# Kernel optimization log

Hardware: AMD Instinct MI355X
Metric: run time of the kernel (lower is better)

The kernel has to match this reference:

```python
import jax, jax.numpy as jnp
import numpy as np

EPS = 1e-5
B, NPB, G = 8, 12500, 64
N = B * NPB
N_EMB, NI, NF = 256, 128, 64
C = NI // 2  # 64


def _bn_relu(x, g, b):
    m = jnp.mean(x, axis=0)
    v = jnp.mean((x - m) ** 2, axis=0)
    return jax.nn.relu(g * (x - m) * jax.lax.rsqrt(v + EPS) + b)


def setup_inputs() -> dict:
    rng = np.random.default_rng(0)
    # unique voxel coords per batch in a 64^3 grid
    coords = np.concatenate([
        np.stack(np.unravel_index(rng.choice(G ** 3, NPB, replace=False), (G, G, G)), axis=1)
        for _ in range(B)
    ], axis=0).astype(np.int64)  # [N,3]
    batch_idx = np.repeat(np.arange(B), NPB).astype(np.int64)
    keys = ((batch_idx * G + coords[:, 0]) * G + coords[:, 1]) * G + coords[:, 2]
    order = np.argsort(keys)
    skeys = keys[order]
    offs = np.array([[dx, dy, dz] for dx in (-1, 0, 1) for dy in (-1, 0, 1) for dz in (-1, 0, 1)], np.int64)
    nbr = np.full((27, N), -1, np.int32)  # rulebook: input idx feeding each output per offset
    for k in range(27):
        nc = coords + offs[k]
        inb = np.all((nc >= 0) & (nc < G), axis=1)
        q = ((batch_idx * G + nc[:, 0]) * G + nc[:, 1]) * G + nc[:, 2]
        pos = np.clip(np.searchsorted(skeys, q), 0, N - 1)
        hit = inb & (skeys[pos] == q)
        nbr[k] = np.where(hit, order[pos], -1).astype(np.int32)

    key = jax.random.key(0)
    ks = jax.random.split(key, 8)
    s1 = 1.0 / np.sqrt(NI)
    s3 = 1.0 / np.sqrt(27 * C)
    su = 1.0 / np.sqrt(C)
    st = 1.0 / np.sqrt(N_EMB)
    return {
        "feats": jax.random.normal(ks[0], (N, NI), jnp.float32),
        "t": jax.random.normal(ks[1], (B, N_EMB), jnp.float32),
        "w_fuse": jax.random.normal(ks[2], (NI, C), jnp.float32) * s1,
        "g1": jnp.ones((C,), jnp.float32), "b1": jnp.zeros((C,), jnp.float32),
        "w_temb": jax.random.normal(ks[3], (N_EMB, C), jnp.float32) * st,
        "b_temb": jnp.zeros((C,), jnp.float32),
        "w3": jax.random.normal(ks[4], (27, C, C), jnp.float32) * s3,
        "g2": jnp.ones((C,), jnp.float32), "b2": jnp.zeros((C,), jnp.float32),
        "wup": jax.random.normal(ks[5], (8, C, NF), jnp.float32) * su,
        "g3": jnp.ones((NF,), jnp.float32), "b3": jnp.zeros((NF,), jnp.float32),
        "batch_idx": jnp.asarray(batch_idx, jnp.int32),
        "nbr": jnp.asarray(nbr),
    }


def reference(feats, t, w_fuse, g1, b1, w_temb, b_temb, w3, g2, b2, wup, g3, b3, batch_idx, nbr):
    # feature_fusion: 1x1 sparse conv == per-point GEMM, then BN + ReLU
    h = _bn_relu(feats @ w_fuse, g1, b1)  # [N, C]
    # time embedding injected per point via batch index
    emb = jax.nn.silu(t) @ w_temb + b_temb  # [B, C]
    h = h + emb[batch_idx]
    # 3x3x3 submanifold sparse conv: gather-GEMM-scatter per kernel offset
    n = h.shape[0]
    out = jnp.zeros_like(h)
    for k in range(nbr.shape[0]):  # fixed 27 offsets
        idx = nbr[k]
        valid = (idx >= 0)[:, None]
        g_k = jnp.where(valid, h[jnp.clip(idx, 0, n - 1)], 0.0)
        out = out + g_k @ w3[k]
    h2 = _bn_relu(out, g2, b2)  # [N, C]
    # transposed conv k=2 s=2: each input spawns 8 unique children -> per-offset GEMM
    up = jnp.einsum('nc,kcf->nkf', h2, wup).reshape(n * wup.shape[0], wup.shape[2])  # [8N, NF]
    return _bn_relu(up, g3, b3)
```

## Files before the change

### kernel.cpp

```cpp
#include <hip/hip_runtime.h>

#define EPSV 1e-5f

typedef __attribute__((ext_vector_type(8))) short short8;
typedef __attribute__((ext_vector_type(4))) short s16x4;
typedef __attribute__((ext_vector_type(4))) float f32x4;
typedef unsigned short ushort_t;

__device__ inline ushort_t f2bf(float f) {
    unsigned int x = __builtin_bit_cast(unsigned int, f);
    unsigned int r = (x + 0x7fffu + ((x >> 16) & 1u)) >> 16;
    return (ushort_t)r;
}
__device__ inline float bf2f(ushort_t u) {
    return __builtin_bit_cast(float, (unsigned int)u << 16);
}

__global__ __launch_bounds__(256) void k_prep(
    const float* __restrict__ w_fuse, const float* __restrict__ w3,
    const float* __restrict__ wup,
    const float* __restrict__ tin, const float* __restrict__ w_temb,
    const float* __restrict__ b_temb, float* __restrict__ emb,
    ushort_t* __restrict__ wfuset2, ushort_t* __restrict__ w3t2,
    ushort_t* __restrict__ wupt, ushort_t* __restrict__ wupt2) {
    if (blockIdx.x == 720) {
        __shared__ float st[8 * 256];
        int t = threadIdx.x;
        for (int i = t; i < 2048; i += 256) { float v = tin[i]; st[i] = v / (1.f + __expf(-v)); }
        __syncthreads();
        for (int p = t; p < 512; p += 256) {
            int bb = p >> 6, c = p & 63;
            float acc = b_temb[c];
            for (int e = 0; e < 256; e++) acc += st[bb * 256 + e] * w_temb[e * 64 + c];
            emb[bb * 64 + c] = acc;
        }
        return;
    }
    int i = blockIdx.x * 256 + threadIdx.x;
    if (i < 8192) {
        int kk = i & 127, ln = (i >> 7) & 15, j = i >> 11;
        wfuset2[i] = f2bf(w_fuse[kk * 64 + 4 * ln + j]);
    } else if (i < 118784) {
        int p = i - 8192;
        int kk = p & 63, ln = (p >> 6) & 15, j = (p >> 10) & 3, k = p >> 12;
        w3t2[p] = f2bf(w3[k * 4096 + kk * 64 + 4 * ln + j]);
    } else if (i < 151552) {
        int p = i - 118784;
        int uk = p >> 12, r = p & 4095, f = r >> 6, c = r & 63;
        wupt[p] = f2bf(wup[uk * 4096 + c * 64 + f]);
    } else if (i < 184320) {
        int p = i - 151552;
        int kk = p & 63, ln = (p >> 6) & 15, j = (p >> 10) & 3, uk = p >> 12;
        wupt2[p] = f2bf(wup[uk * 4096 + kk * 64 + 4 * ln + j]);
    }
}

__global__ __launch_bounds__(256) void k_gemm_fuse(
    const float* __restrict__ feats, const ushort_t* __restrict__ wfuset2,
    ushort_t* __restrict__ T, float* __restrict__ partialT, int npts) {
    __shared__ float sm[4][128];
    int t = threadIdx.x, bid = blockIdx.x;
    int lane = t & 63, w = t >> 6, q = lane >> 4, ln = lane & 15;
    int rbase = bid * 64 + w * 16;
    int row = rbase + ln;
    bool rv = row < npts;
    short8 afr[4];
#pragma unroll
    for (int s = 0; s < 4; s++) {
        short8 v = (short8)0;
        if (rv) {
            const float* src = feats + (size_t)row * 128 + s * 32 + q * 8;
            float4 a = *(const float4*)src;
            float4 b = *(const float4*)(src + 4);
            ushort_t u[8] = {f2bf(a.x), f2bf(a.y), f2bf(a.z), f2bf(a.w),
                             f2bf(b.x), f2bf(b.y), f2bf(b.z), f2bf(b.w)};
            v = *(short8*)u;
        }
        afr[s] = v;
    }
    f32x4 acc[4];
#pragma unroll
    for (int j = 0; j < 4; j++) acc[j] = (f32x4)0.f;
#pragma unroll
    for (int s = 0; s < 4; s++)
#pragma unroll
        for (int j = 0; j < 4; j++) {
            short8 bfr = *(const short8*)&wfuset2[j * 2048 + ln * 128 + s * 32 + q * 8];
            acc[j] = __builtin_amdgcn_mfma_f32_16x16x32_bf16(afr[s], bfr, acc[j], 0, 0, 0);
        }
    float ps[4] = {0, 0, 0, 0}, pq[4] = {0, 0, 0, 0};
#pragma unroll
    for (int r = 0; r < 4; r++) {
        int rr = rbase + q * 4 + r;
        ushort_t o[4];
#pragma unroll
        for (int j = 0; j < 4; j++) {
            float v = acc[j][r];
            ps[j] += v; pq[j] += v * v;
            o[j] = f2bf(v);
        }
        if (rr < npts) *(s16x4*)&T[(size_t)rr * 64 + 4 * ln] = *(s16x4*)o;
    }
#pragma unroll
    for (int j = 0; j < 4; j++) {
        ps[j] += __shfl_xor(ps[j], 16); ps[j] += __shfl_xor(ps[j], 32);
        pq[j] += __shfl_xor(pq[j], 16); pq[j] += __shfl_xor(pq[j], 32);
    }
    if (lane < 16) {
#pragma unroll
        for (int j = 0; j < 4; j++) {
            sm[w][ln * 4 + j] = ps[j];
            sm[w][64 + ln * 4 + j] = pq[j];
        }
    }
    __syncthreads();
    if (t < 128)
        partialT[(size_t)t * 2048 + bid] = sm[0][t] + sm[1][t] + sm[2][t] + sm[3][t];
}

__global__ __launch_bounds__(256) void k_finalize(
    const float* __restrict__ partialT, int nrows, float inv_count,
    const float* __restrict__ g, const float* __restrict__ b, float* __restrict__ prm) {
    int c = blockIdx.x;
    int t = threadIdx.x;
    float S = 0.f, Q = 0.f;
    for (int r = t; r < nrows; r += 256) {
        S += partialT[(size_t)c * 2048 + r];
        Q += partialT[(size_t)(64 + c) * 2048 + r];
    }
#pragma unroll
    for (int d = 1; d < 64; d <<= 1) { S += __shfl_xor(S, d); Q += __shfl_xor(Q, d); }
    __shared__ float sS[4], sQ[4];
    int w = t >> 6;
    if ((t & 63) == 0) { sS[w] = S; sQ[w] = Q; }
    __syncthreads();
    if (t == 0) {
        float s = sS[0] + sS[1] + sS[2] + sS[3];
        float qq = sQ[0] + sQ[1] + sQ[2] + sQ[3];
        float mean = s * inv_count;
        float var = qq * inv_count - mean * mean;
        float scale = g[c] * rsqrtf(var + EPSV);
        prm[c] = scale;
        prm[64 + c] = b[c] - mean * scale;
    }
}

__global__ __launch_bounds__(256) void k_apply1(
    const ushort_t* __restrict__ T, const float* __restrict__ prm,
    const float* __restrict__ emb, const int* __restrict__ bidx,
    ushort_t* __restrict__ h, int npts) {
    int tid = blockIdx.x * 256 + threadIdx.x;
    if (tid >= npts * 8) return;
    int row = tid >> 3, c0 = (tid & 7) * 8;
    int bi = bidx[row];
    short8 x = *(const short8*)&T[(size_t)row * 64 + c0];
    ushort_t o[8];
#pragma unroll
    for (int j = 0; j < 8; j++) {
        int c = c0 + j;
        float v = prm[c] * bf2f((ushort_t)x[j]) + prm[64 + c];
        v = fmaxf(v, 0.f) + emb[bi * 64 + c];
        o[j] = f2bf(v);
    }
    *(short8*)&h[(size_t)row * 64 + c0] = *(short8*)o;
}

__global__ __launch_bounds__(512, 2) void k_conv27(
    const ushort_t* __restrict__ h, const ushort_t* __restrict__ w3t2,
    const int* __restrict__ nbr,
    ushort_t* __restrict__ out2, float* __restrict__ partialT, int npts) {
    __shared__ ushort_t Bl[2][4 * 4096];
    __shared__ float sm[8][128];
    int nwg = gridDim.x;
    int qc = nwg >> 3, rm = nwg & 7;
    int xcd = blockIdx.x & 7, pos = blockIdx.x >> 3;
    int bid = (xcd < rm ? xcd * (qc + 1) : rm * (qc + 1) + (xcd - rm) * qc) + pos;
    int t = threadIdx.x;
    int lane = t & 63, w = t >> 6, q = lane >> 4, ln = lane & 15;
    int rbase = bid * 256 + w * 32;
    int row0 = rbase + ln, row1 = rbase + 16 + ln;
    bool rv0 = row0 < npts, rv1 = row1 < npts;
    int D = t * 16;
    int blk = D >> 10, lane_d = (D >> 4) & 63;
    int srcByte = (blk >> 1) * 2048 + (lane_d & 15) * 128 + (blk & 1) * 64 + (lane_d >> 4) * 16;
    const char* wsrc = (const char*)w3t2 + srcByte;
    char* lbase0 = (char*)&Bl[0][0] + (size_t)w * 1024;
    char* lbase1 = (char*)&Bl[1][0] + (size_t)w * 1024;
#define STAGE(kk, slot, bufp) \
    __builtin_amdgcn_global_load_lds((const unsigned int*)(wsrc + (size_t)(kk) * 8192), \
                                     (unsigned int*)((bufp) + (size_t)(slot) * 8192), 16, 0, 0)
    STAGE(0, 0, lbase0); STAGE(1, 1, lbase0); STAGE(2, 2, lbase0); STAGE(3, 3, lbase0);
    f32x4 acc[2][4];
#pragma unroll
    for (int g = 0; g < 2; g++)
#pragma unroll
        for (int j = 0; j < 4; j++) acc[g][j] = (f32x4)0.f;
    __syncthreads();
#pragma unroll
    for (int c = 0; c < 7; c++) {
        const int nk = (c == 6) ? 3 : 4;
        int id0[4], id1[4];
#pragma unroll
        for (int r = 0; r < 4; r++)
            if (r < nk) {
                int kk = c * 4 + r;
                id0[r] = rv0 ? nbr[(size_t)kk * npts + row0] : -1;
                id1[r] = rv1 ? nbr[(size_t)kk * npts + row1] : -1;
            }
        if (c < 6) {
            const int nkn = (c == 5) ? 3 : 4;
            char* nb = ((c + 1) & 1) ? lbase1 : lbase0;
#pragma unroll
            for (int r = 0; r < 4; r++)
                if (r < nkn) STAGE(4 * (c + 1) + r, r, nb);
        }
        const ushort_t* bl = (c & 1) ? &Bl[1][0] : &Bl[0][0];
#pragma unroll
        for (int r = 0; r < 4; r++) {
            if (r < nk) {
                bool any0 = __any(id0[r] >= 0), any1 = __any(id1[r] >= 0);
                if (any0 || any1) {
                    short8 a00 = (short8)0, a01 = (short8)0;
                    short8 a10 = (short8)0, a11 = (short8)0;
                    if (id0[r] >= 0) {
                        const ushort_t* hp0 = h + (size_t)id0[r] * 64 + q * 8;
                        a00 = *(const short8*)hp0;
                        a01 = *(const short8*)(hp0 + 32);
                    }
                    if (id1[r] >= 0) {
                        const ushort_t* hp1 = h + (size_t)id1[r] * 64 + q * 8;
                        a10 = *(const short8*)hp1;
                        a11 = *(const short8*)(hp1 + 32);
                    }
                    const ushort_t* bt = bl + r * 4096;
#pragma unroll
                    for (int j = 0; j < 4; j++) {
                        short8 b0 = *(const short8*)&bt[(j * 2 + 0) * 512 + lane * 8];
                        short8 b1 = *(const short8*)&bt[(j * 2 + 1) * 512 + lane * 8];
                        if (any0) {
                            acc[0][j] = __builtin_amdgcn_mfma_f32_16x16x32_bf16(a00, b0, acc[0][j], 0, 0, 0);
                            acc[0][j] = __builtin_amdgcn_mfma_f32_16x16x32_bf16(a01, b1, acc[0][j], 0, 0, 0);
                        }
                        if (any1) {
                            acc[1][j] = __builtin_amdgcn_mfma_f32_16x16x32_bf16(a10, b0, acc[1][j], 0, 0, 0);
                            acc[1][j] = __builtin_amdgcn_mfma_f32_16x16x32_bf16(a11, b1, acc[1][j], 0, 0, 0);
                        }
                    }
                }
            }
        }
        __syncthreads();
    }
#undef STAGE
    float ps[4] = {0, 0, 0, 0}, pq[4] = {0, 0, 0, 0};
#pragma unroll
    for (int g = 0; g < 2; g++)
#pragma unroll
        for (int r = 0; r < 4; r++) {
            int rr = rbase + g * 16 + q * 4 + r;
            ushort_t o[4];
#pragma unroll
            for (int j = 0; j < 4; j++) {
                float v = acc[g][j][r];
                ps[j] += v; pq[j] += v * v;
                o[j] = f2bf(v);
            }
            if (rr < npts) *(s16x4*)&out2[(size_t)rr * 64 + 4 * ln] = *(s16x4*)o;
        }
#pragma unroll
    for (int j = 0; j < 4; j++) {
        ps[j] += __shfl_xor(ps[j], 16); ps[j] += __shfl_xor(ps[j], 32);
        pq[j] += __shfl_xor(pq[j], 16); pq[j] += __shfl_xor(pq[j], 32);
    }
    if (lane < 16) {
#pragma unroll
        for (int j = 0; j < 4; j++) {
            sm[w][ln * 4 + j] = ps[j];
            sm[w][64 + ln * 4 + j] = pq[j];
        }
    }
    __syncthreads();
    if (t < 128) {
        float s = 0.f;
#pragma unroll
        for (int i = 0; i < 8; i++) s += sm[i][t];
        partialT[(size_t)t * 2048 + bid] = s;
    }
}

__global__ __launch_bounds__(256) void k_apply2up(
    const ushort_t* __restrict__ out2, const float* __restrict__ prm2,
    const ushort_t* __restrict__ wupt,
    float* __restrict__ partialT, int npts) {
    __shared__ ushort_t A[64 * 72];
    int t = threadIdx.x, bid = blockIdx.x;
    int lane = t & 63, w = t >> 6, q = lane >> 4, ln = lane & 15;
    int nbase = bid * 64;
    for (int i2 = 0; i2 < 2; i2++) {
        int slot = i2 * 256 + t;
        int row = slot >> 3, seg = slot & 7;
        int n = nbase + row;
        short8 val = (short8)0;
        if (n < npts) {
            short8 x = *(const short8*)&out2[(size_t)n * 64 + seg * 8];
            ushort_t o[8];
#pragma unroll
            for (int j = 0; j < 8; j++) {
                int c = seg * 8 + j;
                float v = prm2[c] * bf2f((ushort_t)x[j]) + prm2[64 + c];
                o[j] = f2bf(fmaxf(v, 0.f));
            }
            val = *(short8*)o;
        }
        *(short8*)&A[row * 72 + seg * 8] = val;
    }
    __syncthreads();
    int col = w * 16 + ln;
    short8 afr[4][2];
    for (int i = 0; i < 4; i++)
        for (int s = 0; s < 2; s++)
            afr[i][s] = *(const short8*)&A[(i * 16 + ln) * 72 + s * 32 + q * 8];
    float ps = 0.f, pq = 0.f;
    for (int uk = 0; uk < 8; uk++) {
        f32x4 acc[4];
        for (int i = 0; i < 4; i++) acc[i] = (f32x4)0.f;
        for (int s = 0; s < 2; s++) {
            short8 bfr = *(const short8*)&wupt[(size_t)uk * 4096 + col * 64 + s * 32 + q * 8];
            for (int i = 0; i < 4; i++)
                acc[i] = __builtin_amdgcn_mfma_f32_16x16x32_bf16(afr[i][s], bfr, acc[i], 0, 0, 0);
        }
        for (int i = 0; i < 4; i++)
            for (int r = 0; r < 4; r++) { float v = acc[i][r]; ps += v; pq += v * v; }
    }
    ps += __shfl_xor(ps, 16); ps += __shfl_xor(ps, 32);
    pq += __shfl_xor(pq, 16); pq += __shfl_xor(pq, 32);
    if (lane < 16) {
        partialT[(size_t)col * 2048 + bid] = ps;
        partialT[(size_t)(64 + col) * 2048 + bid] = pq;
    }
}

__global__ __launch_bounds__(512) void k_up(
    const ushort_t* __restrict__ out2, const ushort_t* __restrict__ wupt2,
    const float* __restrict__ prm2, const float* __restrict__ prm3,
    float* __restrict__ outp, int npts) {
    int t = threadIdx.x, bid = blockIdx.x;
    int lane = t & 63, w = t >> 6, q = lane >> 4, ln = lane & 15;
    int rbase = bid * 256 + w * 32;
    short8 afr[2][2];
#pragma unroll
    for (int g = 0; g < 2; g++) {
        int row = rbase + g * 16 + ln;
#pragma unroll
        for (int s = 0; s < 2; s++) {
            short8 v = (short8)0;
            if (row < npts) {
                short8 x = *(const short8*)&out2[(size_t)row * 64 + s * 32 + q * 8];
                ushort_t o[8];
#pragma unroll
                for (int j = 0; j < 8; j++) {
                    int c = s * 32 + q * 8 + j;
                    float vv = prm2[c] * bf2f((ushort_t)x[j]) + prm2[64 + c];
                    o[j] = f2bf(fmaxf(vv, 0.f));
                }
                v = *(short8*)o;
            }
            afr[g][s] = v;
        }
    }
    float4 sc = *(const float4*)&prm3[4 * ln];
    float4 sh = *(const float4*)&prm3[64 + 4 * ln];
    for (int uk = 0; uk < 8; uk++) {
        short8 bfr[2][4];
#pragma unroll
        for (int s = 0; s < 2; s++)
#pragma unroll
            for (int j = 0; j < 4; j++)
                bfr[s][j] = *(const short8*)&wupt2[(size_t)uk * 4096 + j * 1024 + ln * 64 + s * 32 + q * 8];
#pragma unroll
        for (int g = 0; g < 2; g++) {
            f32x4 acc[4];
#pragma unroll
            for (int j = 0; j < 4; j++) acc[j] = (f32x4)0.f;
#pragma unroll
            for (int s = 0; s < 2; s++)
#pragma unroll
                for (int j = 0; j < 4; j++)
                    acc[j] = __builtin_amdgcn_mfma_f32_16x16x32_bf16(afr[g][s], bfr[s][j], acc[j], 0, 0, 0);
#pragma unroll
            for (int r = 0; r < 4; r++) {
                int rr = rbase + g * 16 + q * 4 + r;
                if (rr < npts) {
                    float4 y;
                    y.x = fmaxf(sc.x * acc[0][r] + sh.x, 0.f);
                    y.y = fmaxf(sc.y * acc[1][r] + sh.y, 0.f);
                    y.z = fmaxf(sc.z * acc[2][r] + sh.z, 0.f);
                    y.w = fmaxf(sc.w * acc[3][r] + sh.w, 0.f);
                    *(float4*)&outp[((size_t)rr * 8 + uk) * 64 + 4 * ln] = y;
                }
            }
        }
    }
}

extern "C" void kernel_launch(void* const* d_in, const int* in_sizes, int n_in,
                              void* d_out, int out_size, void* d_ws, size_t ws_size,
                              hipStream_t stream) {
    const float* feats  = (const float*)d_in[0];
    const float* tin    = (const float*)d_in[1];
    const float* w_fuse = (const float*)d_in[2];
    const float* g1     = (const float*)d_in[3];
    const float* b1     = (const float*)d_in[4];
    const float* w_temb = (const float*)d_in[5];
    const float* b_temb = (const float*)d_in[6];
    const float* w3     = (const float*)d_in[7];
    const float* g2     = (const float*)d_in[8];
    const float* b2     = (const float*)d_in[9];
    const float* wup    = (const float*)d_in[10];
    const float* g3     = (const float*)d_in[11];
    const float* b3     = (const float*)d_in[12];
    const int* bidx     = (const int*)d_in[13];
    const int* nbr      = (const int*)d_in[14];

    int npts = in_sizes[13];
    float* dout = (float*)d_out;

    char* ob = (char*)d_out;
    ushort_t* T     = (ushort_t*)ob;
    ushort_t* h     = (ushort_t*)(ob + (size_t)npts * 128);
    ushort_t* out2  = (ushort_t*)(ob + (size_t)npts * 256);

    char* ws = (char*)d_ws;
    float* partialT   = (float*)ws;
    float* prm        = (float*)(ws + 1048576);
    float* emb        = (float*)(ws + 1048576 + 4096);
    ushort_t* wfuset2 = (ushort_t*)(ws + 1048576 + 8192);
    ushort_t* w3t2    = (ushort_t*)(ws + 1048576 + 8192 + 16384);
    ushort_t* wupt    = (ushort_t*)(ws + 1048576 + 8192 + 16384 + 221184);
    ushort_t* wupt2   = (ushort_t*)(ws + 1048576 + 8192 + 16384 + 221184 + 65536);

    int nblk  = (npts + 63) / 64;
    int nblk3 = (npts + 255) / 256;
    int napp  = (npts * 8 + 255) / 256;

    k_prep<<<721, 256, 0, stream>>>(w_fuse, w3, wup, tin, w_temb, b_temb, emb,
                                    wfuset2, w3t2, wupt, wupt2);
    k_gemm_fuse<<<nblk, 256, 0, stream>>>(feats, wfuset2, T, partialT, npts);
    k_finalize<<<64, 256, 0, stream>>>(partialT, nblk, 1.f / npts, g1, b1, prm);
    k_apply1<<<napp, 256, 0, stream>>>(T, prm, emb, bidx, h, npts);
    k_conv27<<<nblk3, 512, 0, stream>>>(h, w3t2, nbr, out2, partialT, npts);
    k_finalize<<<64, 256, 0, stream>>>(partialT, nblk3, 1.f / npts, g2, b2, prm + 128);
    k_apply2up<<<nblk, 256, 0, stream>>>(out2, prm + 128, wupt, partialT, npts);
    k_finalize<<<64, 256, 0, stream>>>(partialT, nblk, 1.f / (8.f * npts), g3, b3, prm + 256);
    k_up<<<nblk3, 512, 0, stream>>>(out2, wupt2, prm + 128, prm + 256, dout, npts);
}
```

Measured before the change: 161.8 us.

## Fuse BN1, ReLU and time-embedding add into conv27 neighbor gather

Removes the k_apply1 pass. k_conv27 now gathers raw T rows and applies the BN1 scale/shift, ReLU and time-embedding add on the fly, with the per-channel constants and embedding staged in LDS. The batch index comes from a magic-number division that assumes every batch has the same number of points, so batch_idx is no longer read. This saves writing and re-reading the intermediate h tensor and one kernel launch, in exchange for redoing the elementwise math on every neighbor gather. Smaller changes: the occupancy hint rises to 4, the final output uses nontemporal stores, and out2 moves into the workspace.

```diff
diff --git a/kernel.cpp b/kernel.cpp
--- a/kernel.cpp
+++ b/kernel.cpp
@@ -145,37 +145,54 @@
     }
 }
 
-__global__ __launch_bounds__(256) void k_apply1(
-    const ushort_t* __restrict__ T, const float* __restrict__ prm,
-    const float* __restrict__ emb, const int* __restrict__ bidx,
-    ushort_t* __restrict__ h, int npts) {
-    int tid = blockIdx.x * 256 + threadIdx.x;
-    if (tid >= npts * 8) return;
-    int row = tid >> 3, c0 = (tid & 7) * 8;
-    int bi = bidx[row];
-    short8 x = *(const short8*)&T[(size_t)row * 64 + c0];
-    ushort_t o[8];
-#pragma unroll
-    for (int j = 0; j < 8; j++) {
-        int c = c0 + j;
-        float v = prm[c] * bf2f((ushort_t)x[j]) + prm[64 + c];
-        v = fmaxf(v, 0.f) + emb[bi * 64 + c];
-        o[j] = f2bf(v);
-    }
-    *(short8*)&h[(size_t)row * 64 + c0] = *(short8*)o;
-}
-
-__global__ __launch_bounds__(512, 2) void k_conv27(
-    const ushort_t* __restrict__ h, const ushort_t* __restrict__ w3t2,
-    const int* __restrict__ nbr,
+__device__ inline void gbn(const ushort_t* __restrict__ T, int id, int q,
+                           const float* cst, unsigned int magicM,
+                           short8& a0, short8& a1) {
+    a0 = (short8)0; a1 = (short8)0;
+    if (id >= 0) {
+        const ushort_t* tp = T + (size_t)id * 64 + q * 8;
+        short8 x0 = *(const short8*)tp;
+        short8 x1 = *(const short8*)(tp + 32);
+        unsigned int bi = __umulhi((unsigned int)id, magicM);
+        const float* eb = cst + 128 + bi * 64 + q * 8;
+        float sa[8], ha[8], sb[8], hb[8], e0[8], e1[8];
+        *(float4*)&sa[0] = *(const float4*)&cst[q * 8];
+        *(float4*)&sa[4] = *(const float4*)&cst[q * 8 + 4];
+        *(float4*)&ha[0] = *(const float4*)&cst[64 + q * 8];
+        *(float4*)&ha[4] = *(const float4*)&cst[64 + q * 8 + 4];
+        *(float4*)&sb[0] = *(const float4*)&cst[32 + q * 8];
+        *(float4*)&sb[4] = *(const float4*)&cst[32 + q * 8 + 4];
+        *(float4*)&hb[0] = *(const float4*)&cst[96 + q * 8];
+        *(float4*)&hb[4] = *(const float4*)&cst[96 + q * 8 + 4];
+        *(float4*)&e0[0] = *(const float4*)eb;
+        *(float4*)&e0[4] = *(const float4*)(eb + 4);
+        *(float4*)&e1[0] = *(const float4*)(eb + 32);
+        *(float4*)&e1[4] = *(const float4*)(eb + 36);
+        ushort_t o0[8], o1[8];
+#pragma unroll
+        for (int j = 0; j < 8; j++) {
+            o0[j] = f2bf(fmaxf(sa[j] * bf2f((ushort_t)x0[j]) + ha[j], 0.f) + e0[j]);
+            o1[j] = f2bf(fmaxf(sb[j] * bf2f((ushort_t)x1[j]) + hb[j], 0.f) + e1[j]);
+        }
+        a0 = *(short8*)o0; a1 = *(short8*)o1;
+    }
+}
+
+__global__ __launch_bounds__(512, 4) void k_conv27(
+    const ushort_t* __restrict__ T, const ushort_t* __restrict__ w3t2,
+    const int* __restrict__ nbr, const float* __restrict__ prm1,
+    const float* __restrict__ emb, unsigned int magicM,
     ushort_t* __restrict__ out2, float* __restrict__ partialT, int npts) {
     __shared__ ushort_t Bl[2][4 * 4096];
     __shared__ float sm[8][128];
+    __shared__ float cst[640];
     int nwg = gridDim.x;
     int qc = nwg >> 3, rm = nwg & 7;
     int xcd = blockIdx.x & 7, pos = blockIdx.x >> 3;
     int bid = (xcd < rm ? xcd * (qc + 1) : rm * (qc + 1) + (xcd - rm) * qc) + pos;
     int t = threadIdx.x;
+    if (t < 128) cst[t] = prm1[t];
+    if (t < 512) cst[128 + t] = emb[t];
     int lane = t & 63, w = t >> 6, q = lane >> 4, ln = lane & 15;
     int rbase = bid * 256 + w * 32;
     int row0 = rbase + ln, row1 = rbase + 16 + ln;
@@ -220,18 +237,9 @@
             if (r < nk) {
                 bool any0 = __any(id0[r] >= 0), any1 = __any(id1[r] >= 0);
                 if (any0 || any1) {
-                    short8 a00 = (short8)0, a01 = (short8)0;
-                    short8 a10 = (short8)0, a11 = (short8)0;
-                    if (id0[r] >= 0) {
-                        const ushort_t* hp0 = h + (size_t)id0[r] * 64 + q * 8;
-                        a00 = *(const short8*)hp0;
-                        a01 = *(const short8*)(hp0 + 32);
-                    }
-                    if (id1[r] >= 0) {
-                        const ushort_t* hp1 = h + (size_t)id1[r] * 64 + q * 8;
-                        a10 = *(const short8*)hp1;
-                        a11 = *(const short8*)(hp1 + 32);
-                    }
+                    short8 a00, a01, a10, a11;
+                    gbn(T, id0[r], q, cst, magicM, a00, a01);
+                    gbn(T, id1[r], q, cst, magicM, a10, a11);
                     const ushort_t* bt = bl + r * 4096;
 #pragma unroll
                     for (int j = 0; j < 4; j++) {
@@ -391,12 +399,12 @@
             for (int r = 0; r < 4; r++) {
                 int rr = rbase + g * 16 + q * 4 + r;
                 if (rr < npts) {
-                    float4 y;
-                    y.x = fmaxf(sc.x * acc[0][r] + sh.x, 0.f);
-                    y.y = fmaxf(sc.y * acc[1][r] + sh.y, 0.f);
-                    y.z = fmaxf(sc.z * acc[2][r] + sh.z, 0.f);
-                    y.w = fmaxf(sc.w * acc[3][r] + sh.w, 0.f);
-                    *(float4*)&outp[((size_t)rr * 8 + uk) * 64 + 4 * ln] = y;
+                    f32x4 y;
+                    y[0] = fmaxf(sc.x * acc[0][r] + sh.x, 0.f);
+                    y[1] = fmaxf(sc.y * acc[1][r] + sh.y, 0.f);
+                    y[2] = fmaxf(sc.z * acc[2][r] + sh.z, 0.f);
+                    y[3] = fmaxf(sc.w * acc[3][r] + sh.w, 0.f);
+                    __builtin_nontemporal_store(y, (f32x4*)&outp[((size_t)rr * 8 + uk) * 64 + 4 * ln]);
                 }
             }
         }
@@ -419,16 +427,15 @@
     const float* wup    = (const float*)d_in[10];
     const float* g3     = (const float*)d_in[11];
     const float* b3     = (const float*)d_in[12];
-    const int* bidx     = (const int*)d_in[13];
     const int* nbr      = (const int*)d_in[14];
 
     int npts = in_sizes[13];
+    int Bn   = in_sizes[1] / 256;
+    int NPB  = npts / Bn;
+    unsigned int magicM = (unsigned int)(((1ULL << 32) + (unsigned)NPB - 1) / (unsigned)NPB);
     float* dout = (float*)d_out;
 
-    char* ob = (char*)d_out;
-    ushort_t* T     = (ushort_t*)ob;
-    ushort_t* h     = (ushort_t*)(ob + (size_t)npts * 128);
-    ushort_t* out2  = (ushort_t*)(ob + (size_t)npts * 256);
+    ushort_t* T = (ushort_t*)d_out;
 
     char* ws = (char*)d_ws;
     float* partialT   = (float*)ws;
@@ -438,17 +445,16 @@
     ushort_t* w3t2    = (ushort_t*)(ws + 1048576 + 8192 + 16384);
     ushort_t* wupt    = (ushort_t*)(ws + 1048576 + 8192 + 16384 + 221184);
     ushort_t* wupt2   = (ushort_t*)(ws + 1048576 + 8192 + 16384 + 221184 + 65536);
+    ushort_t* out2    = (ushort_t*)(ws + 1048576 + 8192 + 16384 + 221184 + 131072);
 
     int nblk  = (npts + 63) / 64;
     int nblk3 = (npts + 255) / 256;
-    int napp  = (npts * 8 + 255) / 256;
 
     k_prep<<<721, 256, 0, stream>>>(w_fuse, w3, wup, tin, w_temb, b_temb, emb,
                                     wfuset2, w3t2, wupt, wupt2);
     k_gemm_fuse<<<nblk, 256, 0, stream>>>(feats, wfuset2, T, partialT, npts);
     k_finalize<<<64, 256, 0, stream>>>(partialT, nblk, 1.f / npts, g1, b1, prm);
-    k_apply1<<<napp, 256, 0, stream>>>(T, prm, emb, bidx, h, npts);
-    k_conv27<<<nblk3, 512, 0, stream>>>(h, w3t2, nbr, out2, partialT, npts);
+    k_conv27<<<nblk3, 512, 0, stream>>>(T, w3t2, nbr, prm, emb, magicM, out2, partialT, npts);
     k_finalize<<<64, 256, 0, stream>>>(partialT, nblk3, 1.f / npts, g2, b2, prm + 128);
     k_apply2up<<<nblk, 256, 0, stream>>>(out2, prm + 128, wupt, partialT, npts);
     k_finalize<<<64, 256, 0, stream>>>(partialT, nblk, 1.f / (8.f * npts), g3, b3, prm + 256);
```

Result: slower. 173.8 us (+7.4%).
